# Kernel tuning notes

Measured on AMD Instinct MI355X. Metric: run time of the kernel, lower is better.

Reference implementation:

```python
import jax, jax.numpy as jnp
import numpy as np

# FP8 E4M3 constants (per FP8Handler)
E4M3_MAX = 240.0          # max_normal
MANTISSA_SCALE = 8.0      # 2 ** mantissa_bits (3)
SCALE_EPS = 1e-10


def setup_inputs() -> dict:
    key = jax.random.key(0)
    k1, k2, k3 = jax.random.split(key, 3)
    B, S, D_IN, D_OUT = 4, 2048, 4096, 4096
    x = jax.random.normal(k1, (B, S, D_IN), dtype=jnp.float32)
    weight = jax.random.normal(k2, (D_OUT, D_IN), dtype=jnp.float32)
    bias = jax.random.normal(k3, (D_OUT,), dtype=jnp.float32)
    return {"x": x, "weight": weight, "bias": bias}


def _fp8_e4m3_quant_dequant(w, scale):
    # FP8Handler.quantize_tensor + _simulate_e4m3_precision
    s = jnp.clip(w / scale, -E4M3_MAX, E4M3_MAX)
    s = s.astype(jnp.float16).astype(jnp.float32)  # fp16 round-trip
    q = jnp.round(s * MANTISSA_SCALE) / MANTISSA_SCALE  # mantissa truncation
    q = jnp.clip(q, -E4M3_MAX, E4M3_MAX)
    return q * scale


def reference(x, weight, bias):
    # FP8Quantizer.compute_scale: per-tensor max-abs, margin=0, fresh history
    amax = jnp.max(jnp.abs(weight))
    scale = jnp.maximum(amax / E4M3_MAX, SCALE_EPS)
    qw = _fp8_e4m3_quant_dequant(weight, scale)  # [out, in]
    # F.linear(x, qw, bias): x [b, s, in] @ qw.T [in, out] + bias
    return jnp.einsum('bsi,oi->bso', x, qw) + bias
```

## Files before the change

kernel.cpp:

```cpp
#include <hip/hip_runtime.h>
#include <hip/hip_bf16.h>
#include <hip/hip_fp16.h>

#define E4M3_MAX 240.0f

typedef __attribute__((ext_vector_type(8))) __bf16 bf16x8;
typedef __attribute__((ext_vector_type(4))) float f32x4;
typedef unsigned short ushort_t;

__device__ __forceinline__ void gload_lds16(const void* g, void* l) {
  __builtin_amdgcn_global_load_lds(
      (const __attribute__((address_space(1))) void*)g,
      (__attribute__((address_space(3))) void*)l,
      16, 0, 0);
}

__global__ void amax_abs_kernel(const float* __restrict__ w, int n4,
                                unsigned* __restrict__ amax_bits) {
  float m = 0.0f;
  const float4* w4 = (const float4*)w;
  int stride = gridDim.x * blockDim.x;
  for (int i = blockIdx.x * blockDim.x + threadIdx.x; i < n4; i += stride) {
    float4 v = w4[i];
    m = fmaxf(m, fmaxf(fmaxf(fabsf(v.x), fabsf(v.y)),
                       fmaxf(fabsf(v.z), fabsf(v.w))));
  }
  for (int off = 32; off > 0; off >>= 1)
    m = fmaxf(m, __shfl_down(m, off, 64));
  __shared__ float smax[4];
  int l = threadIdx.x & 63, wv = threadIdx.x >> 6;
  if (l == 0) smax[wv] = m;
  __syncthreads();
  if (threadIdx.x == 0) {
    float bm = fmaxf(fmaxf(smax[0], smax[1]), fmaxf(smax[2], smax[3]));
    atomicMax(amax_bits, __float_as_uint(bm));
  }
}

__global__ void quant_weight_kernel(const float* __restrict__ w,
                                    const unsigned* __restrict__ amax_bits,
                                    ushort_t* __restrict__ qw, int n4) {
  float amax = __uint_as_float(*amax_bits);
  float scale = fmaxf(amax / E4M3_MAX, 1e-10f);
  const float4* w4 = (const float4*)w;
  ushort4* q4 = (ushort4*)qw;
  int stride = gridDim.x * blockDim.x;
  for (int i = blockIdx.x * blockDim.x + threadIdx.x; i < n4; i += stride) {
    float4 v = w4[i];
    float r[4] = {v.x, v.y, v.z, v.w};
    ushort_t o[4];
#pragma unroll
    for (int j = 0; j < 4; ++j) {
      float s = fminf(fmaxf(r[j] / scale, -E4M3_MAX), E4M3_MAX);
      s = __half2float(__float2half(s));
      float q = rintf(s * 8.0f) * 0.125f;
      q = fminf(fmaxf(q, -E4M3_MAX), E4M3_MAX);
      __hip_bfloat16 h = __float2bfloat16(q * scale);
      o[j] = *(ushort_t*)&h;
    }
    ushort4 ov = {o[0], o[1], o[2], o[3]};
    q4[i] = ov;
  }
}

__global__ void cvt_bf16_kernel(const float* __restrict__ x,
                                ushort_t* __restrict__ xb, int n4) {
  const float4* x4 = (const float4*)x;
  ushort4* o4 = (ushort4*)xb;
  int stride = gridDim.x * blockDim.x;
  for (int i = blockIdx.x * blockDim.x + threadIdx.x; i < n4; i += stride) {
    float4 v = x4[i];
    __hip_bfloat16 h0 = __float2bfloat16(v.x);
    __hip_bfloat16 h1 = __float2bfloat16(v.y);
    __hip_bfloat16 h2 = __float2bfloat16(v.z);
    __hip_bfloat16 h3 = __float2bfloat16(v.w);
    ushort4 o = {*(ushort_t*)&h0, *(ushort_t*)&h1,
                 *(ushort_t*)&h2, *(ushort_t*)&h3};
    o4[i] = o;
  }
}


#define BAR() do { asm volatile("" ::: "memory"); \
                   __builtin_amdgcn_s_barrier(); \
                   asm volatile("" ::: "memory"); } while (0)
#define LGKM(n) do { asm volatile("s_waitcnt lgkmcnt(" #n ")" ::: "memory"); \
                     __builtin_amdgcn_sched_barrier(0); } while (0)
#define VMC(n)  do { asm volatile("s_waitcnt vmcnt(" #n ")" ::: "memory"); \
                     __builtin_amdgcn_sched_barrier(0); } while (0)

__global__ __launch_bounds__(512, 2) void gemm256_pipe(
    const ushort_t* __restrict__ A, const ushort_t* __restrict__ Bt,
    const float* __restrict__ bias, float* __restrict__ C) {
  constexpr int K = 4096, N = 4096;
  __shared__ __align__(16) ushort_t As[2][2][8192];
  __shared__ __align__(16) ushort_t Bs[2][2][8192];

  const int tid = threadIdx.x;
  const int wid = tid >> 6, lane = tid & 63;
  const int wm = wid >> 2, wn = wid & 3;
  const int lk = lane >> 4, lr = lane & 15;

  int bid = blockIdx.x;
  int swz = (bid & 7) * 64 + (bid >> 3);
  int bm = swz >> 4, bn = swz & 15;

  const ushort_t* Ab = A + (size_t)bm * 256 * K;
  const ushort_t* Bb = Bt + (size_t)bn * 256 * K;

  int offG[2];
#pragma unroll
  for (int q = 0; q < 2; ++q) {
    int s = q * 512 + tid;
    int row = s >> 3;
    int c = (s & 7) ^ (row & 7);
    offG[q] = row * K + c * 8;
  }

#define STAGE_A2(buf, kt)                                                  \
  do { _Pragma("unroll") for (int h = 0; h < 2; ++h)                       \
    _Pragma("unroll") for (int q = 0; q < 2; ++q)                          \
      gload_lds16(Ab + (size_t)h * 128 * K + (kt) * 64 + offG[q],          \
                  &As[buf][h][(q * 512 + wid * 64) * 8]); } while (0)
#define STAGE_B2(buf, kt)                                                  \
  do { _Pragma("unroll") for (int h = 0; h < 2; ++h)                       \
    _Pragma("unroll") for (int q = 0; q < 2; ++q)                          \
      gload_lds16(Bb + (size_t)h * 128 * K + (kt) * 64 + offG[q],          \
                  &Bs[buf][h][(q * 512 + wid * 64) * 8]); } while (0)

  const int abase = lr * 64;
  const int bbase = (wn & 1) * 4096 + lr * 64;
  const int bhalf = wn >> 1;
  const int xk0 = ((lk) ^ (lr & 7)) * 8;
  const int xk1 = ((4 + lk) ^ (lr & 7)) * 8;

  bf16x8 afX[4], afY[4], bfE[4], bfO[4];
  f32x4 acc[8][4] = {};

#define RD_A(dst, buf, fi0, xkv)                                           \
  do { _Pragma("unroll") for (int i = 0; i < 4; ++i)                       \
    dst[i] = *(const bf16x8*)&As[buf][wm][abase + ((fi0) + i) * 1024 + (xkv)]; } while (0)
#define RD_B4(dst, buf, xkv)                                               \
  do { _Pragma("unroll") for (int j = 0; j < 4; ++j)                       \
    dst[j] = *(const bf16x8*)&Bs[buf][bhalf][bbase + j * 1024 + (xkv)]; } while (0)
#define RD_B2(dst, j0, buf, xkv)                                           \
  do { _Pragma("unroll") for (int j = 0; j < 2; ++j)                       \
    dst[(j0) + j] = *(const bf16x8*)&Bs[buf][bhalf][bbase + ((j0) + j) * 1024 + (xkv)]; } while (0)

#define MMA(areg, breg, H)                                                 \
  do { __builtin_amdgcn_s_setprio(1);                                      \
    _Pragma("unroll") for (int i = 0; i < 4; ++i)                          \
      _Pragma("unroll") for (int j = 0; j < 4; ++j)                        \
        acc[(H) * 4 + i][j] = __builtin_amdgcn_mfma_f32_16x16x32_bf16(     \
            areg[i], breg[j], acc[(H) * 4 + i][j], 0, 0, 0);               \
    __builtin_amdgcn_s_setprio(0);                                         \
    __builtin_amdgcn_sched_barrier(0); } while (0)

#define TILE(buf, obuf, t, DO_SA, DO_SB, LAST)                             \
  do {                                                                     \
    RD_A(afY, buf, 4, xk0); RD_B2(bfO, 0, buf, xk1);                       \
    if (DO_SA) STAGE_A2(obuf, (t) + 1);                                    \
    LGKM(6); MMA(afX, bfE, 0); BAR();                                      \
    RD_A(afX, buf, 0, xk1); RD_B2(bfO, 2, buf, xk1);                       \
    LGKM(6); MMA(afY, bfE, 1); BAR();                                      \
    RD_A(afY, buf, 4, xk1);                                                \
    LGKM(4); MMA(afX, bfO, 0); VMC(0); BAR();                              \
    if (!(LAST)) { RD_A(afX, obuf, 0, xk0); RD_B4(bfE, obuf, xk0); }       \
    if (DO_SB) STAGE_B2(buf, (t) + 2);                                     \
    if (!(LAST)) { LGKM(8); MMA(afY, bfO, 1); BAR(); }                     \
    else         { LGKM(0); MMA(afY, bfO, 1); }                            \
  } while (0)

  STAGE_A2(0, 0); STAGE_B2(0, 0);
  STAGE_B2(1, 1);
  VMC(4);
  BAR();
  RD_A(afX, 0, 0, xk0); RD_B4(bfE, 0, xk0);

  for (int t = 0; t < 62; t += 2) {
    TILE(0, 1, t, 1, 1, 0);
    TILE(1, 0, t + 1, 1, 1, 0);
  }
  TILE(0, 1, 62, 1, 0, 0);
  TILE(1, 0, 63, 0, 0, 1);

  float* Cb = C + (size_t)(bm * 256 + wm * 128) * N + bn * 256 + wn * 64;
#pragma unroll
  for (int fj = 0; fj < 4; ++fj) {
    int n = fj * 16 + lr;
    float bv = bias[bn * 256 + wn * 64 + n];
#pragma unroll
    for (int fi = 0; fi < 8; ++fi) {
      int m0 = fi * 16 + lk * 4;
#pragma unroll
      for (int r = 0; r < 4; ++r)
        Cb[(size_t)(m0 + r) * N + n] = acc[fi][fj][r] + bv;
    }
  }
}

extern "C" void kernel_launch(void* const* d_in, const int* in_sizes, int n_in,
                              void* d_out, int out_size, void* d_ws, size_t ws_size,
                              hipStream_t stream) {
  const float* x = (const float*)d_in[0];
  const float* wt = (const float*)d_in[1];
  const float* bias = (const float*)d_in[2];
  float* out = (float*)d_out;

  const int DIN = 4096;
  const int NW = in_sizes[1];
  const int M = in_sizes[0] / DIN;

  char* ws = (char*)d_ws;
  unsigned* amax_bits = (unsigned*)ws;
  ushort_t* qw = (ushort_t*)(ws + 256);
  ushort_t* xb = (ushort_t*)(ws + 256 + (size_t)NW * 2);

  hipMemsetAsync(amax_bits, 0, 4, stream);
  hipLaunchKernelGGL(amax_abs_kernel, dim3(1024), dim3(256), 0, stream,
                     wt, NW / 4, amax_bits);
  hipLaunchKernelGGL(quant_weight_kernel, dim3(2048), dim3(256), 0, stream,
                     wt, amax_bits, qw, NW / 4);
  hipLaunchKernelGGL(cvt_bf16_kernel, dim3(2048), dim3(256), 0, stream,
                     x, xb, (M * DIN) / 4);

  hipLaunchKernelGGL(gemm256_pipe, dim3(512), dim3(512), 0, stream,
                     xb, qw, bias, out);
}
```

Before: 364.9 us.

## Rebalance GEMM main loop into eight uniform read-stage-MMA phases

```diff
diff --git a/kernel.cpp b/kernel.cpp
--- a/kernel.cpp
+++ b/kernel.cpp
@@ -84,12 +84,13 @@
 #define BAR() do { asm volatile("" ::: "memory"); \
                    __builtin_amdgcn_s_barrier(); \
                    asm volatile("" ::: "memory"); } while (0)
-#define LGKM(n) do { asm volatile("s_waitcnt lgkmcnt(" #n ")" ::: "memory"); \
+#define LGKM0() do { asm volatile("s_waitcnt lgkmcnt(0)" ::: "memory"); \
                      __builtin_amdgcn_sched_barrier(0); } while (0)
-#define VMC(n)  do { asm volatile("s_waitcnt vmcnt(" #n ")" ::: "memory"); \
-                     __builtin_amdgcn_sched_barrier(0); } while (0)
-
-__global__ __launch_bounds__(512, 2) void gemm256_pipe(
+#define VMC4() asm volatile("s_waitcnt vmcnt(4)" ::: "memory")
+#define VMC0() asm volatile("s_waitcnt vmcnt(0)" ::: "memory")
+#define NOVM() do {} while (0)
+
+__global__ __launch_bounds__(512, 2) void gemm256_bal(
     const ushort_t* __restrict__ A, const ushort_t* __restrict__ Bt,
     const float* __restrict__ bias, float* __restrict__ C) {
   constexpr int K = 4096, N = 4096;
@@ -117,16 +118,14 @@
     offG[q] = row * K + c * 8;
   }
 
-#define STAGE_A2(buf, kt)                                                  \
-  do { _Pragma("unroll") for (int h = 0; h < 2; ++h)                       \
-    _Pragma("unroll") for (int q = 0; q < 2; ++q)                          \
-      gload_lds16(Ab + (size_t)h * 128 * K + (kt) * 64 + offG[q],          \
-                  &As[buf][h][(q * 512 + wid * 64) * 8]); } while (0)
-#define STAGE_B2(buf, kt)                                                  \
-  do { _Pragma("unroll") for (int h = 0; h < 2; ++h)                       \
-    _Pragma("unroll") for (int q = 0; q < 2; ++q)                          \
-      gload_lds16(Bb + (size_t)h * 128 * K + (kt) * 64 + offG[q],          \
-                  &Bs[buf][h][(q * 512 + wid * 64) * 8]); } while (0)
+#define STAGE_AH(buf, kt, h)                                               \
+  do { _Pragma("unroll") for (int q = 0; q < 2; ++q)                       \
+    gload_lds16(Ab + (size_t)(h) * 128 * K + (kt) * 64 + offG[q],          \
+                &As[buf][h][(q * 512 + wid * 64) * 8]); } while (0)
+#define STAGE_BH(buf, kt, h)                                               \
+  do { _Pragma("unroll") for (int q = 0; q < 2; ++q)                       \
+    gload_lds16(Bb + (size_t)(h) * 128 * K + (kt) * 64 + offG[q],          \
+                &Bs[buf][h][(q * 512 + wid * 64) * 8]); } while (0)
 
   const int abase = lr * 64;
   const int bbase = (wn & 1) * 4096 + lr * 64;
@@ -134,55 +133,62 @@
   const int xk0 = ((lk) ^ (lr & 7)) * 8;
   const int xk1 = ((4 + lk) ^ (lr & 7)) * 8;
 
-  bf16x8 afX[4], afY[4], bfE[4], bfO[4];
+  bf16x8 afA[4], afB[4], bfK0[4], bfK1[4];
   f32x4 acc[8][4] = {};
 
-#define RD_A(dst, buf, fi0, xkv)                                           \
+#define RD_A4(dst, buf, fi0, xkv)                                          \
   do { _Pragma("unroll") for (int i = 0; i < 4; ++i)                       \
     dst[i] = *(const bf16x8*)&As[buf][wm][abase + ((fi0) + i) * 1024 + (xkv)]; } while (0)
-#define RD_B4(dst, buf, xkv)                                               \
+#define RD_B4K(dst, buf, xkv)                                              \
   do { _Pragma("unroll") for (int j = 0; j < 4; ++j)                       \
     dst[j] = *(const bf16x8*)&Bs[buf][bhalf][bbase + j * 1024 + (xkv)]; } while (0)
-#define RD_B2(dst, j0, buf, xkv)                                           \
-  do { _Pragma("unroll") for (int j = 0; j < 2; ++j)                       \
-    dst[(j0) + j] = *(const bf16x8*)&Bs[buf][bhalf][bbase + ((j0) + j) * 1024 + (xkv)]; } while (0)
-
-#define MMA(areg, breg, H)                                                 \
+
+#define MMA16(areg, breg, FI0)                                             \
   do { __builtin_amdgcn_s_setprio(1);                                      \
     _Pragma("unroll") for (int i = 0; i < 4; ++i)                          \
       _Pragma("unroll") for (int j = 0; j < 4; ++j)                        \
-        acc[(H) * 4 + i][j] = __builtin_amdgcn_mfma_f32_16x16x32_bf16(     \
-            areg[i], breg[j], acc[(H) * 4 + i][j], 0, 0, 0);               \
-    __builtin_amdgcn_s_setprio(0);                                         \
-    __builtin_amdgcn_sched_barrier(0); } while (0)
-
-#define TILE(buf, obuf, t, DO_SA, DO_SB, LAST)                             \
+        acc[(FI0) + i][j] = __builtin_amdgcn_mfma_f32_16x16x32_bf16(       \
+            areg[i], breg[j], acc[(FI0) + i][j], 0, 0, 0);                 \
+    __builtin_amdgcn_s_setprio(0); } while (0)
+
+#define ITER(t, SA1, SB2, SA2, SB3, VM4K, VM8K)                            \
   do {                                                                     \
-    RD_A(afY, buf, 4, xk0); RD_B2(bfO, 0, buf, xk1);                       \
-    if (DO_SA) STAGE_A2(obuf, (t) + 1);                                    \
-    LGKM(6); MMA(afX, bfE, 0); BAR();                                      \
-    RD_A(afX, buf, 0, xk1); RD_B2(bfO, 2, buf, xk1);                       \
-    LGKM(6); MMA(afY, bfE, 1); BAR();                                      \
-    RD_A(afY, buf, 4, xk1);                                                \
-    LGKM(4); MMA(afX, bfO, 0); VMC(0); BAR();                              \
-    if (!(LAST)) { RD_A(afX, obuf, 0, xk0); RD_B4(bfE, obuf, xk0); }       \
-    if (DO_SB) STAGE_B2(buf, (t) + 2);                                     \
-    if (!(LAST)) { LGKM(8); MMA(afY, bfO, 1); BAR(); }                     \
-    else         { LGKM(0); MMA(afY, bfO, 1); }                            \
+    RD_B4K(bfK0, 0, xk0); RD_A4(afA, 0, 0, xk0);                           \
+    if (SA1) STAGE_AH(1, (t) + 1, 0);                                      \
+    BAR(); LGKM0(); MMA16(afA, bfK0, 0); BAR();                            \
+    RD_B4K(bfK1, 0, xk1); RD_A4(afB, 0, 4, xk0);                           \
+    if (SA1) STAGE_AH(1, (t) + 1, 1);                                      \
+    BAR(); LGKM0(); MMA16(afB, bfK0, 4); BAR();                            \
+    RD_A4(afA, 0, 0, xk1);                                                 \
+    if (SB2) STAGE_BH(0, (t) + 2, 0);                                      \
+    BAR(); LGKM0(); MMA16(afA, bfK1, 0); BAR();                            \
+    RD_A4(afB, 0, 4, xk1);                                                 \
+    if (SB2) STAGE_BH(0, (t) + 2, 1);                                      \
+    BAR(); LGKM0(); MMA16(afB, bfK1, 4); VM4K; BAR();                      \
+    RD_B4K(bfK0, 1, xk0); RD_A4(afA, 1, 0, xk0);                           \
+    if (SA2) STAGE_AH(0, (t) + 2, 0);                                      \
+    BAR(); LGKM0(); MMA16(afA, bfK0, 0); BAR();                            \
+    RD_B4K(bfK1, 1, xk1); RD_A4(afB, 1, 4, xk0);                           \
+    if (SA2) STAGE_AH(0, (t) + 2, 1);                                      \
+    BAR(); LGKM0(); MMA16(afB, bfK0, 4); BAR();                            \
+    RD_A4(afA, 1, 0, xk1);                                                 \
+    if (SB3) STAGE_BH(1, (t) + 3, 0);                                      \
+    BAR(); LGKM0(); MMA16(afA, bfK1, 0); BAR();                            \
+    RD_A4(afB, 1, 4, xk1);                                                 \
+    if (SB3) STAGE_BH(1, (t) + 3, 1);                                      \
+    BAR(); LGKM0(); MMA16(afB, bfK1, 4); VM8K; BAR();                      \
   } while (0)
 
-  STAGE_A2(0, 0); STAGE_B2(0, 0);
-  STAGE_B2(1, 1);
-  VMC(4);
+  STAGE_AH(0, 0, 0); STAGE_AH(0, 0, 1);
+  STAGE_BH(0, 0, 0); STAGE_BH(0, 0, 1);
+  STAGE_BH(1, 1, 0); STAGE_BH(1, 1, 1);
+  VMC4();
   BAR();
-  RD_A(afX, 0, 0, xk0); RD_B4(bfE, 0, xk0);
-
-  for (int t = 0; t < 62; t += 2) {
-    TILE(0, 1, t, 1, 1, 0);
-    TILE(1, 0, t + 1, 1, 1, 0);
-  }
-  TILE(0, 1, 62, 1, 0, 0);
-  TILE(1, 0, 63, 0, 0, 1);
+
+  for (int t = 0; t < 62; t += 2)
+    ITER(t, 1, (t) < 62 - 0, 1, 1, VMC4(), VMC4());
+
+  ITER(62, 1, 0, 0, 0, VMC0(), NOVM());
 
   float* Cb = C + (size_t)(bm * 256 + wm * 128) * N + bn * 256 + wn * 64;
 #pragma unroll
@@ -224,6 +230,6 @@
   hipLaunchKernelGGL(cvt_bf16_kernel, dim3(2048), dim3(256), 0, stream,
                      x, xb, (M * DIN) / 4);
 
-  hipLaunchKernelGGL(gemm256_pipe, dim3(512), dim3(512), 0, stream,
+  hipLaunchKernelGGL(gemm256_bal, dim3(512), dim3(512), 0, stream,
                      xb, qw, bias, out);
 }
```

Result: slower. 383.5 us (+5.1%).
